# Optimization experiments

Measured on AMD Instinct MI355X. Metric: run time of the kernel, lower is better.

The kernel has to match this reference:

```python
import jax, jax.numpy as jnp
import numpy as np

T, B = 128, 512
OBS_DIM = 512
HIDDEN = 512
ACTION_DIM = 18
LN_EPS = 1e-6  # flax LayerNorm default


def _layer_norm(x, scale, bias):
    m = jnp.mean(x, axis=-1, keepdims=True)
    v = jnp.var(x, axis=-1, keepdims=True)
    return (x - m) * jax.lax.rsqrt(v + LN_EPS) * scale + bias


def setup_inputs() -> dict:
    key = jax.random.key(0)
    ks = jax.random.split(key, 16)
    sc = lambda k, sh: jax.random.normal(k, sh, jnp.float32) * (1.0 / np.sqrt(sh[0]))
    d = {}
    d['hidden'] = jax.random.normal(ks[0], (B, HIDDEN), jnp.float32)
    d['obs'] = jax.random.normal(ks[1], (T, B, OBS_DIM), jnp.float32)
    d['dones'] = jax.random.randint(ks[2], (T, B), 0, 2).astype(bool)
    d['last_acts'] = jax.random.randint(ks[3], (T, B), 0, ACTION_DIM, dtype=jnp.int32)
    in0 = OBS_DIM + ACTION_DIM
    d['w0'] = sc(ks[4], (in0, HIDDEN)); d['b0'] = jnp.zeros((HIDDEN,), jnp.float32)
    d['ln0_s'] = jnp.ones((HIDDEN,), jnp.float32); d['ln0_b'] = jnp.zeros((HIDDEN,), jnp.float32)
    d['w1'] = sc(ks[5], (HIDDEN, HIDDEN)); d['b1'] = jnp.zeros((HIDDEN,), jnp.float32)
    d['ln1_s'] = jnp.ones((HIDDEN,), jnp.float32); d['ln1_b'] = jnp.zeros((HIDDEN,), jnp.float32)
    d['w_ir'] = sc(ks[6], (HIDDEN, HIDDEN)); d['b_ir'] = jnp.zeros((HIDDEN,), jnp.float32)
    d['w_iz'] = sc(ks[7], (HIDDEN, HIDDEN)); d['b_iz'] = jnp.zeros((HIDDEN,), jnp.float32)
    d['w_in'] = sc(ks[8], (HIDDEN, HIDDEN)); d['b_in'] = jnp.zeros((HIDDEN,), jnp.float32)
    d['w_hr'] = sc(ks[9], (HIDDEN, HIDDEN))
    d['w_hz'] = sc(ks[10], (HIDDEN, HIDDEN))
    d['w_hn'] = sc(ks[11], (HIDDEN, HIDDEN)); d['b_hn'] = jnp.zeros((HIDDEN,), jnp.float32)
    d['w_out'] = sc(ks[12], (HIDDEN, ACTION_DIM)); d['b_out'] = jnp.zeros((ACTION_DIM,), jnp.float32)
    return d


def reference(hidden, obs, dones, last_acts,
              w0, b0, ln0_s, ln0_b, w1, b1, ln1_s, ln1_b,
              w_ir, b_ir, w_iz, b_iz, w_in, b_in,
              w_hr, w_hz, w_hn, b_hn, w_out, b_out):
    # embed last actions and concat with obs: [T, B, obs_dim + action_dim]
    one_hot = jax.nn.one_hot(last_acts, ACTION_DIM, dtype=obs.dtype)
    x = jnp.concatenate([obs, one_hot], axis=-1)
    # MLP encoder: Dense -> LayerNorm -> relu, applied over all (T, B) at once
    x = jax.nn.relu(_layer_norm(x @ w0 + b0, ln0_s, ln0_b))
    x = jax.nn.relu(_layer_norm(x @ w1 + b1, ln1_s, ln1_b))

    # ScannedRNN: GRUCell with reset-to-zero carry on done, scanned over time
    def step(h, xs):
        xt, dt = xs  # xt: [B, H], dt: [B] bool
        h = jnp.where(dt[:, None], jnp.zeros_like(h), h)
        r = jax.nn.sigmoid(xt @ w_ir + b_ir + h @ w_hr)
        z = jax.nn.sigmoid(xt @ w_iz + b_iz + h @ w_hz)
        n = jnp.tanh(xt @ w_in + b_in + r * (h @ w_hn + b_hn))
        h_new = (1.0 - z) * n + z * h
        return h_new, h_new

    new_hidden, y = jax.lax.scan(step, hidden, (x, dones))
    q_vals = y @ w_out + b_out  # [T, B, action_dim]
    return new_hidden, q_vals
```

## Files before the change

### kernel.cpp

```cpp
#include <hip/hip_runtime.h>
#include <cstdint>
#include <cstddef>


#define TT 128
#define BBATCH 512
#define HH 512
#define MM 65536
#define AD 18

typedef __attribute__((ext_vector_type(8))) short short8;
typedef __attribute__((ext_vector_type(4))) float float4v;
typedef __attribute__((ext_vector_type(4))) unsigned int uint4v;

__device__ __forceinline__ unsigned short f2bf(float f) {
  union { float f; unsigned int u; } v; v.f = f;
  unsigned int r = v.u + 0x7fffu + ((v.u >> 16) & 1u);
  return (unsigned short)(r >> 16);
}
__device__ __forceinline__ float bf2f(unsigned short h) {
  union { unsigned int u; float f; } v; v.u = ((unsigned int)h) << 16;
  return v.f;
}

__device__ __forceinline__ unsigned int load_u32_coh(const unsigned int* p) {
  unsigned int v;
  asm volatile("global_load_dword %0, %1, off sc0 sc1\n\ts_waitcnt vmcnt(0)"
               : "=v"(v) : "v"(p) : "memory");
  return v;
}
__device__ __forceinline__ void store_u32_coh(unsigned int* p, unsigned int v) {
  asm volatile("global_store_dword %0, %1, off sc0 sc1"
               :: "v"(p), "v"(v) : "memory");
}
__device__ __forceinline__ void store_u16_coh(unsigned short* p, unsigned int v) {
  asm volatile("global_store_short %0, %1, off sc0 sc1"
               :: "v"(p), "v"(v) : "memory");
}

typedef __attribute__((address_space(3))) unsigned int* lds_u32p;
typedef const __attribute__((address_space(1))) unsigned int* glb_u32p;
__device__ __forceinline__ void async16(void* lds, const void* g) {
  __builtin_amdgcn_global_load_lds(
      (glb_u32p)(unsigned long long)g,
      (lds_u32p)(unsigned int)(unsigned long long)lds, 16, 0, 0);
}


__global__ __launch_bounds__(256) void k_conv_obs(
    const float* __restrict__ src, unsigned short* __restrict__ dst,
    unsigned int* __restrict__ flag) {
  if (blockIdx.x == 0 && threadIdx.x == 0) *flag = 0u;
  int i = blockIdx.x * 256 + threadIdx.x;
  float4v v = ((const float4v*)src)[i];
  unsigned long long pk = (unsigned long long)f2bf(v[0])
      | ((unsigned long long)f2bf(v[1]) << 16)
      | ((unsigned long long)f2bf(v[2]) << 32)
      | ((unsigned long long)f2bf(v[3]) << 48);
  ((unsigned long long*)dst)[i] = pk;
}

__global__ __launch_bounds__(256) void k_prep_t(
    const float* __restrict__ w0, const float* __restrict__ w1,
    const float* __restrict__ wir, const float* __restrict__ wiz,
    const float* __restrict__ win,
    unsigned short* __restrict__ W0at, unsigned short* __restrict__ W1t,
    unsigned short* __restrict__ Wit) {
  int o = blockIdx.x * 256 + threadIdx.x;
  int n = o >> 9, k = o & 511;
  int z = blockIdx.y;
  const float* s = (z == 0) ? w0 : (z == 1) ? w1 : (z == 2) ? wir
                 : (z == 3) ? wiz : win;
  unsigned short b = f2bf(s[k * 512 + n]);
  if (z == 0) W0at[o] = b;
  else if (z == 1) W1t[o] = b;
  else Wit[(size_t)(z - 2) * 262144 + o] = b;
}

__global__ __launch_bounds__(256) void k_prep_whf(
    const float* __restrict__ whr, const float* __restrict__ whz,
    const float* __restrict__ whn, unsigned short* __restrict__ Whf) {
  int i = blockIdx.x * 256 + threadIdx.x;
  int k = i / 1536, n = i - k * 1536;
  const float* s = (n < 512) ? whr : (n < 1024) ? whz : whn;
  float v = s[k * 512 + (n & 511)];
  Whf[((size_t)(k >> 3) * 1536 + n) * 8 + (k & 7)] = f2bf(v);
}

__global__ __launch_bounds__(256) void k_prep_misc(
    const float* __restrict__ w0, const float* __restrict__ bir,
    const float* __restrict__ biz, const float* __restrict__ bin,
    const float* __restrict__ wout, const float* __restrict__ hidden,
    const int* __restrict__ dI,
    unsigned short* __restrict__ w0act, float* __restrict__ gib,
    unsigned short* __restrict__ WoutT, unsigned short* __restrict__ hbuf,
    unsigned int* __restrict__ ready, unsigned int* __restrict__ flag) {
  int i = blockIdx.x * 256 + threadIdx.x;
  if (i < 9216) {
    int a = i >> 9, n = i & 511;
    w0act[i] = f2bf(w0[(512 + a) * 512 + n]);
  }
  if (i < 1536)
    gib[i] = (i < 512) ? bir[i] : (i < 1024) ? biz[i - 512] : bin[i - 1024];
  if (i < 32768) {
    int n = i >> 9, k = i & 511;
    WoutT[i] = f2bf(n < AD ? wout[k * AD + n] : 0.f);
  }
  if (i < 262144) hbuf[i] = f2bf(hidden[i]);
  if (i < 33280) ready[i] = 0u;
  if (i < 16384) { if (dI[i] & 0xFFFFFFFE) atomicOr(flag, 1u); }
}


template <int MODE>
__global__ __launch_bounds__(256) void k_gemm_bt(
    const unsigned short* __restrict__ Ab,
    const unsigned short* __restrict__ Btb,
    unsigned short* __restrict__ Cb,
    int Ndim, const float* __restrict__ bias,
    const unsigned short* __restrict__ gW,
    const int* __restrict__ acts) {
  __shared__ unsigned short As[4096];
  __shared__ unsigned short Bs[4096];
  const int tid = threadIdx.x, wave = tid >> 6, lane = tid & 63;
  const int quad = lane >> 4, l15 = lane & 15;
  const int m0 = blockIdx.x * 128, n0 = blockIdx.y * 128;
  const int mblk = (wave & 1) * 64, nblk = (wave >> 1) * 64;

  float4v acc[4][4];
#pragma unroll
  for (int a = 0; a < 4; ++a)
#pragma unroll
    for (int b = 0; b < 4; ++b) acc[a][b] = (float4v){0.f, 0.f, 0.f, 0.f};

  for (int k0 = 0; k0 < 512; k0 += 32) {
#pragma unroll
    for (int r = 0; r < 2; ++r) {
      int u = r * 256 + wave * 64 + lane;
      int ch = u >> 7, mm = u & 127;
      async16(&As[(size_t)(r * 256 + wave * 64) * 8],
              Ab + (size_t)(m0 + mm) * 512 + k0 + ch * 8);
      async16(&Bs[(size_t)(r * 256 + wave * 64) * 8],
              Btb + (size_t)(n0 + mm) * 512 + k0 + ch * 8);
    }
    __syncthreads();
    short8 afr[4], bfr[4];
#pragma unroll
    for (int mi = 0; mi < 4; ++mi)
      afr[mi] = *(const short8*)&As[((quad << 7) + mblk + mi * 16 + l15) * 8];
#pragma unroll
    for (int ni = 0; ni < 4; ++ni)
      bfr[ni] = *(const short8*)&Bs[((quad << 7) + nblk + ni * 16 + l15) * 8];
#pragma unroll
    for (int mi = 0; mi < 4; ++mi)
#pragma unroll
      for (int ni = 0; ni < 4; ++ni)
        acc[mi][ni] = __builtin_amdgcn_mfma_f32_16x16x32_bf16(
            afr[mi], bfr[ni], acc[mi][ni], 0, 0, 0);
    __syncthreads();
  }

#pragma unroll
  for (int mi = 0; mi < 4; ++mi) {
#pragma unroll
    for (int i = 0; i < 4; ++i) {
      int row = m0 + mblk + mi * 16 + quad * 4 + i;
      int arow = (MODE == 1) ? acts[row] : 0;
#pragma unroll
      for (int ni = 0; ni < 4; ++ni) {
        int col = n0 + nblk + ni * 16 + l15;
        float v = acc[mi][ni][i] + bias[col];
        if (MODE == 1) v += bf2f(gW[arow * 512 + col]);
        Cb[(size_t)row * Ndim + col] = f2bf(v);
      }
    }
  }
}


__global__ __launch_bounds__(256) void k_ln_relu(
    const unsigned short* __restrict__ X, unsigned short* __restrict__ Y,
    const float* __restrict__ sc, const float* __restrict__ bi) {
  int row = blockIdx.x * 4 + (threadIdx.x >> 6);
  int lane = threadIdx.x & 63;
  uint4v u = *(const uint4v*)(X + (size_t)row * 512 + lane * 8);
  float v[8];
#pragma unroll
  for (int j = 0; j < 4; ++j) {
    v[2 * j] = bf2f((unsigned short)(u[j] & 0xffffu));
    v[2 * j + 1] = bf2f((unsigned short)(u[j] >> 16));
  }
  float s = 0.f, q = 0.f;
#pragma unroll
  for (int j = 0; j < 8; ++j) { s += v[j]; q += v[j] * v[j]; }
#pragma unroll
  for (int d = 1; d < 64; d <<= 1) {
    s += __shfl_xor(s, d, 64);
    q += __shfl_xor(q, d, 64);
  }
  float mean = s * (1.f / 512.f);
  float var = fmaxf(q * (1.f / 512.f) - mean * mean, 0.f);
  float rstd = rsqrtf(var + 1e-6f);
  float4v s0 = *(const float4v*)(sc + lane * 8);
  float4v s1 = *(const float4v*)(sc + lane * 8 + 4);
  float4v c0 = *(const float4v*)(bi + lane * 8);
  float4v c1 = *(const float4v*)(bi + lane * 8 + 4);
  uint4v w;
#pragma unroll
  for (int j = 0; j < 4; ++j) {
    float a0 = fmaxf((v[2 * j] - mean) * rstd * (j < 2 ? s0[2 * j] : s1[2 * j - 4])
                         + (j < 2 ? c0[2 * j] : c1[2 * j - 4]), 0.f);
    float a1 = fmaxf((v[2 * j + 1] - mean) * rstd
                         * (j < 2 ? s0[2 * j + 1] : s1[2 * j - 3])
                         + (j < 2 ? c0[2 * j + 1] : c1[2 * j - 3]), 0.f);
    w[j] = (unsigned int)f2bf(a0) | ((unsigned int)f2bf(a1) << 16);
  }
  *(uint4v*)(Y + (size_t)row * 512 + lane * 8) = w;
}


__global__ __launch_bounds__(256, 1) void k_gru(
    const unsigned short* __restrict__ Whf, const unsigned short* __restrict__ gin,
    const float* __restrict__ bhn, const int* __restrict__ dI,
    const unsigned char* __restrict__ dB, const unsigned int* __restrict__ flag,
    const unsigned short* __restrict__ hbuf, unsigned short* __restrict__ ybuf,
    float* __restrict__ outh, unsigned int* __restrict__ ready) {
  const int tid = threadIdx.x, wave = tid >> 6, lane = tid & 63;
  const int quad = lane >> 4, l15 = lane & 15;
  const int rt = blockIdx.x & 7;
  const int cc = blockIdx.x >> 3;
  const int r0 = rt * 64 + wave * 16;
  const int col = cc * 16 + l15;
  const int bytemode = (int)(*flag);
  const float bhn_c = bhn[col];

  short8 bw[3][16];
#pragma unroll
  for (int kc = 0; kc < 16; ++kc)
#pragma unroll
    for (int g = 0; g < 3; ++g) {
      size_t u = (size_t)(kc * 4 + quad) * 1536 + (g * 512 + col);
      bw[g][kc] = *(const short8*)(Whf + u * 8);
    }

  float hprev[4];
#pragma unroll
  for (int i = 0; i < 4; ++i) {
    int row = r0 + quad * 4 + i;
    hprev[i] = bf2f(hbuf[(size_t)row * 512 + col]);
  }

  const int myrowA = r0 + l15;

  float ginr[4], ginz[4], ginn[4];
  int dd[4], dA;
  {
    const unsigned short* gbase = gin;
#pragma unroll
    for (int i = 0; i < 4; ++i) {
      int row = r0 + quad * 4 + i;
      dd[i] = bytemode ? (int)dB[row] : dI[row];
      ginr[i] = bf2f(gbase[(size_t)row * 1536 + col]);
      ginz[i] = bf2f(gbase[(size_t)row * 1536 + 512 + col]);
      ginn[i] = bf2f(gbase[(size_t)row * 1536 + 1024 + col]);
    }
    dA = bytemode ? (int)dB[myrowA] : dI[myrowA];
  }

  for (int t = 0; t < TT; ++t) {
    if (t > 0) {
      if (wave == 0) {
        const unsigned int* fp =
            ready + ((size_t)rt * 130 + t) * 32 + (lane & 31);
        unsigned int v;
        int guard = 0;
        do {
          v = load_u32_coh(fp);
        } while (__ballot(v == 0u) != 0ull && ++guard < (1 << 22));
      }
      __syncthreads();
      asm volatile("" ::: "memory");
    }

    const unsigned short* hsrc =
        (t == 0) ? hbuf : ybuf + (size_t)(t - 1) * 262144;
    const unsigned short* ap = hsrc + (size_t)myrowA * 512 + quad * 8;
    short8 af[16];
#pragma unroll
    for (int kc = 0; kc < 16; ++kc) af[kc] = *(const short8*)(ap + kc * 32);
    if (dA) {
      const short8 z8 = {0, 0, 0, 0, 0, 0, 0, 0};
#pragma unroll
      for (int kc = 0; kc < 16; ++kc) af[kc] = z8;
    }

    float4v a0 = {0.f, 0.f, 0.f, 0.f}, a1 = a0, a2 = a0;
#pragma unroll
    for (int kc = 0; kc < 16; ++kc) {
      a0 = __builtin_amdgcn_mfma_f32_16x16x32_bf16(af[kc], bw[0][kc], a0, 0, 0, 0);
      a1 = __builtin_amdgcn_mfma_f32_16x16x32_bf16(af[kc], bw[1][kc], a1, 0, 0, 0);
      a2 = __builtin_amdgcn_mfma_f32_16x16x32_bf16(af[kc], bw[2][kc], a2, 0, 0, 0);
    }

    unsigned short* ydst = ybuf + (size_t)t * 262144;
#pragma unroll
    for (int i = 0; i < 4; ++i) {
      int row = r0 + quad * 4 + i;
      float hold = dd[i] ? 0.f : hprev[i];
      float r = 1.f / (1.f + __expf(-(a0[i] + ginr[i])));
      float z = 1.f / (1.f + __expf(-(a1[i] + ginz[i])));
      float npre = ginn[i] + r * (a2[i] + bhn_c);
      float n = 1.f - 2.f / (1.f + __expf(2.f * npre));
      float hnew = (1.f - z) * n + z * hold;
      hprev[i] = hnew;
      store_u16_coh(ydst + (size_t)row * 512 + col, (unsigned int)f2bf(hnew));
      if (t == TT - 1) outh[(size_t)row * 512 + col] = hnew;
    }

    __syncthreads();
    if (tid == 0)
      store_u32_coh(&ready[((size_t)rt * 130 + t + 1) * 32 + cc], 1u);

    if (t < TT - 1) {
      int tn = t + 1;
      const unsigned short* gbase = gin + (size_t)tn * 512 * 1536;
#pragma unroll
      for (int i = 0; i < 4; ++i) {
        int row = r0 + quad * 4 + i;
        dd[i] = bytemode ? (int)dB[tn * 512 + row] : dI[tn * 512 + row];
        ginr[i] = bf2f(gbase[(size_t)row * 1536 + col]);
        ginz[i] = bf2f(gbase[(size_t)row * 1536 + 512 + col]);
        ginn[i] = bf2f(gbase[(size_t)row * 1536 + 1024 + col]);
      }
      dA = bytemode ? (int)dB[tn * 512 + myrowA] : dI[tn * 512 + myrowA];
    }
  }
}


__global__ __launch_bounds__(256) void k_qout(
    const unsigned short* __restrict__ Yb, const unsigned short* __restrict__ Wt,
    const float* __restrict__ bout, float* __restrict__ Q) {
  __shared__ unsigned short As[4096];
  __shared__ unsigned short Bs[2048];
  const int tid = threadIdx.x, wave = tid >> 6, lane = tid & 63;
  const int quad = lane >> 4, l15 = lane & 15;
  const int m0 = blockIdx.x * 128;

  float4v acc[2][4];
#pragma unroll
  for (int a = 0; a < 2; ++a)
#pragma unroll
    for (int b = 0; b < 4; ++b) acc[a][b] = (float4v){0.f, 0.f, 0.f, 0.f};

  for (int k0 = 0; k0 < 512; k0 += 32) {
#pragma unroll
    for (int r = 0; r < 2; ++r) {
      int u = r * 256 + wave * 64 + lane;
      int ch = u >> 7, mm = u & 127;
      async16(&As[(size_t)(r * 256 + wave * 64) * 8],
              Yb + (size_t)(m0 + mm) * 512 + k0 + ch * 8);
    }
    {
      int u = wave * 64 + lane;
      int ch = u >> 6, nn = u & 63;
      async16(&Bs[(size_t)(wave * 64) * 8], Wt + (size_t)nn * 512 + k0 + ch * 8);
    }
    __syncthreads();
    short8 afr[2], bfr[4];
#pragma unroll
    for (int mi = 0; mi < 2; ++mi)
      afr[mi] = *(const short8*)&As[((quad << 7) + wave * 32 + mi * 16 + l15) * 8];
#pragma unroll
    for (int ni = 0; ni < 4; ++ni)
      bfr[ni] = *(const short8*)&Bs[((quad << 6) + ni * 16 + l15) * 8];
#pragma unroll
    for (int mi = 0; mi < 2; ++mi)
#pragma unroll
      for (int ni = 0; ni < 4; ++ni)
        acc[mi][ni] = __builtin_amdgcn_mfma_f32_16x16x32_bf16(
            afr[mi], bfr[ni], acc[mi][ni], 0, 0, 0);
    __syncthreads();
  }
#pragma unroll
  for (int mi = 0; mi < 2; ++mi)
#pragma unroll
    for (int ni = 0; ni < 4; ++ni)
#pragma unroll
      for (int i = 0; i < 4; ++i) {
        int row = m0 + wave * 32 + mi * 16 + quad * 4 + i;
        int colq = ni * 16 + l15;
        if (colq < AD) Q[(size_t)row * AD + colq] = acc[mi][ni][i] + bout[colq];
      }
}


extern "C" void kernel_launch(void* const* d_in, const int* in_sizes, int n_in,
                              void* d_out, int out_size, void* d_ws,
                              size_t ws_size, hipStream_t stream) {
  const float* hidden = (const float*)d_in[0];
  const float* obs = (const float*)d_in[1];
  const void* dones = d_in[2];
  const int* acts = (const int*)d_in[3];
  const float* w0 = (const float*)d_in[4];
  const float* b0 = (const float*)d_in[5];
  const float* ln0s = (const float*)d_in[6];
  const float* ln0b = (const float*)d_in[7];
  const float* w1 = (const float*)d_in[8];
  const float* b1 = (const float*)d_in[9];
  const float* ln1s = (const float*)d_in[10];
  const float* ln1b = (const float*)d_in[11];
  const float* wir = (const float*)d_in[12];
  const float* bir = (const float*)d_in[13];
  const float* wiz = (const float*)d_in[14];
  const float* biz = (const float*)d_in[15];
  const float* win = (const float*)d_in[16];
  const float* bin = (const float*)d_in[17];
  const float* whr = (const float*)d_in[18];
  const float* whz = (const float*)d_in[19];
  const float* whn = (const float*)d_in[20];
  const float* bhn = (const float*)d_in[21];
  const float* wout = (const float*)d_in[22];
  const float* bout = (const float*)d_in[23];

  char* ws = (char*)d_ws;
  unsigned short* bufA = (unsigned short*)(ws);
  unsigned short* bufB = (unsigned short*)(ws + 67108864ULL);
  unsigned short* gin = (unsigned short*)(ws + 134217728ULL);
  char* D = ws + 134217728ULL + 201326592ULL;
  unsigned short* W0at = (unsigned short*)(D);
  unsigned short* W1t = (unsigned short*)(D + 524288);
  unsigned short* Wit = (unsigned short*)(D + 1048576);
  unsigned short* Whf = (unsigned short*)(D + 2621440);
  unsigned short* WoutT = (unsigned short*)(D + 4194304);
  unsigned short* w0act = (unsigned short*)(D + 4259840);
  float* gib = (float*)(D + 4292608);
  unsigned short* hbuf = (unsigned short*)(D + 4300800);
  unsigned int* ready = (unsigned int*)(D + 5349376);
  unsigned int* flag = ready + 33280;

  (void)in_sizes; (void)n_in; (void)out_size; (void)ws_size;

  k_conv_obs<<<32768, 256, 0, stream>>>(obs, bufA, flag);
  k_prep_t<<<dim3(1024, 5), 256, 0, stream>>>(w0, w1, wir, wiz, win, W0at, W1t, Wit);
  k_prep_whf<<<3072, 256, 0, stream>>>(whr, whz, whn, Whf);
  k_prep_misc<<<1024, 256, 0, stream>>>(w0, bir, biz, bin, wout, hidden,
                                        (const int*)dones, w0act, gib, WoutT,
                                        hbuf, ready, flag);
  k_gemm_bt<1><<<dim3(512, 4), 256, 0, stream>>>(bufA, W0at, bufB, 512, b0, w0act, acts);
  k_ln_relu<<<16384, 256, 0, stream>>>(bufB, bufA, ln0s, ln0b);
  k_gemm_bt<0><<<dim3(512, 4), 256, 0, stream>>>(bufA, W1t, bufB, 512, b1, nullptr, nullptr);
  k_ln_relu<<<16384, 256, 0, stream>>>(bufB, bufA, ln1s, ln1b);
  k_gemm_bt<0><<<dim3(512, 12), 256, 0, stream>>>(bufA, Wit, gin, 1536, gib, nullptr, nullptr);
  k_gru<<<256, 256, 0, stream>>>(Whf, gin, bhn, (const int*)dones,
                                 (const unsigned char*)dones, flag, hbuf, bufB,
                                 (float*)d_out, ready);
  k_qout<<<512, 256, 0, stream>>>(bufB, WoutT, bout, (float*)d_out + 262144);
}
```

Measured before the change: 1.363 ms.

## Stage GRU input gates into LDS asynchronously and transpose MFMA for packed stores

```diff
diff --git a/kernel.cpp b/kernel.cpp
--- a/kernel.cpp
+++ b/kernel.cpp
@@ -8,6 +8,7 @@
 #define HH 512
 #define MM 65536
 #define AD 18
+#define GSTEPS 4
 
 typedef __attribute__((ext_vector_type(8))) short short8;
 typedef __attribute__((ext_vector_type(4))) float float4v;
@@ -33,8 +34,8 @@
   asm volatile("global_store_dword %0, %1, off sc0 sc1"
                :: "v"(p), "v"(v) : "memory");
 }
-__device__ __forceinline__ void store_u16_coh(unsigned short* p, unsigned int v) {
-  asm volatile("global_store_short %0, %1, off sc0 sc1"
+__device__ __forceinline__ void store_u64_coh(void* p, unsigned long long v) {
+  asm volatile("global_store_dwordx2 %0, %1, off sc0 sc1"
                :: "v"(p), "v"(v) : "memory");
 }
 
@@ -225,47 +226,64 @@
     const unsigned char* __restrict__ dB, const unsigned int* __restrict__ flag,
     const unsigned short* __restrict__ hbuf, unsigned short* __restrict__ ybuf,
     float* __restrict__ outh, unsigned int* __restrict__ ready) {
+  __shared__ __align__(16) unsigned short gin_lds[2][GSTEPS * 3 * 64 * 16];
+  __shared__ unsigned char d_lds[TT * 64];
+
   const int tid = threadIdx.x, wave = tid >> 6, lane = tid & 63;
   const int quad = lane >> 4, l15 = lane & 15;
   const int rt = blockIdx.x & 7;
   const int cc = blockIdx.x >> 3;
-  const int r0 = rt * 64 + wave * 16;
-  const int col = cc * 16 + l15;
+  const int r0b = rt * 64;
+  const int rowb = wave * 16 + l15;
+  const int row = r0b + rowb;
+  const int c0 = cc * 16 + quad * 4;
   const int bytemode = (int)(*flag);
-  const float bhn_c = bhn[col];
+  const float4v bhn4 = *(const float4v*)(bhn + c0);
+
+  auto stage_gin = [&](int buf, int t0) {
+#pragma unroll
+    for (int r = 0; r < 6; ++r) {
+      int u = r * 256 + tid;
+      int half = u & 1;
+      int v = u >> 1;
+      int rr = v & 63;
+      int v2 = v >> 6;
+      int g = v2 % 3, s = v2 / 3;
+      const unsigned short* src = gin
+          + ((size_t)(t0 + s) * 512 + r0b + rr) * 1536 + g * 512 + cc * 16
+          + half * 8;
+      async16(&gin_lds[buf][(size_t)(r * 256 + wave * 64) * 8], src);
+    }
+  };
+
+  stage_gin(0, 0);
+#pragma unroll
+  for (int r = 0; r < 32; ++r) {
+    int idx = r * 256 + tid;
+    int t = idx >> 6, rr = idx & 63;
+    int gidx = t * 512 + r0b + rr;
+    d_lds[idx] = bytemode ? dB[gidx] : (unsigned char)(dI[gidx] != 0);
+  }
 
   short8 bw[3][16];
 #pragma unroll
   for (int kc = 0; kc < 16; ++kc)
 #pragma unroll
     for (int g = 0; g < 3; ++g) {
-      size_t u = (size_t)(kc * 4 + quad) * 1536 + (g * 512 + col);
+      size_t u = (size_t)(kc * 4 + quad) * 1536 + (g * 512 + cc * 16 + l15);
       bw[g][kc] = *(const short8*)(Whf + u * 8);
     }
 
   float hprev[4];
-#pragma unroll
-  for (int i = 0; i < 4; ++i) {
-    int row = r0 + quad * 4 + i;
-    hprev[i] = bf2f(hbuf[(size_t)row * 512 + col]);
-  }
-
-  const int myrowA = r0 + l15;
-
-  float ginr[4], ginz[4], ginn[4];
-  int dd[4], dA;
   {
-    const unsigned short* gbase = gin;
-#pragma unroll
-    for (int i = 0; i < 4; ++i) {
-      int row = r0 + quad * 4 + i;
-      dd[i] = bytemode ? (int)dB[row] : dI[row];
-      ginr[i] = bf2f(gbase[(size_t)row * 1536 + col]);
-      ginz[i] = bf2f(gbase[(size_t)row * 1536 + 512 + col]);
-      ginn[i] = bf2f(gbase[(size_t)row * 1536 + 1024 + col]);
-    }
-    dA = bytemode ? (int)dB[myrowA] : dI[myrowA];
-  }
+    unsigned long long w = *(const unsigned long long*)(hbuf + (size_t)row * 512 + c0);
+#pragma unroll
+    for (int i = 0; i < 4; ++i) hprev[i] = bf2f((unsigned short)(w >> (16 * i)));
+  }
+
+  __syncthreads();
+
+  const unsigned short* apOffBase = nullptr;  (void)apOffBase;
 
   for (int t = 0; t < TT; ++t) {
     if (t > 0) {
@@ -284,56 +302,72 @@
 
     const unsigned short* hsrc =
         (t == 0) ? hbuf : ybuf + (size_t)(t - 1) * 262144;
-    const unsigned short* ap = hsrc + (size_t)myrowA * 512 + quad * 8;
+    const unsigned short* ap = hsrc + (size_t)row * 512 + quad * 8;
     short8 af[16];
 #pragma unroll
     for (int kc = 0; kc < 16; ++kc) af[kc] = *(const short8*)(ap + kc * 32);
-    if (dA) {
+
+    const int dd = (int)d_lds[(t << 6) + rowb];
+    if (dd) {
       const short8 z8 = {0, 0, 0, 0, 0, 0, 0, 0};
 #pragma unroll
       for (int kc = 0; kc < 16; ++kc) af[kc] = z8;
     }
 
+    if ((t & (GSTEPS - 1)) == 0 && t + GSTEPS < TT)
+      stage_gin(((t >> 2) + 1) & 1, t + GSTEPS);
+
+    const int sl = t & (GSTEPS - 1), bufc = (t >> 2) & 1;
+    float gr[4], gz[4], gn[4];
+    {
+      const unsigned short* gl =
+          &gin_lds[bufc][((size_t)(sl * 3) * 64 + rowb) * 16 + quad * 4];
+      unsigned long long w0 = *(const unsigned long long*)(gl);
+      unsigned long long w1 = *(const unsigned long long*)(gl + 1024);
+      unsigned long long w2 = *(const unsigned long long*)(gl + 2048);
+#pragma unroll
+      for (int i = 0; i < 4; ++i) {
+        gr[i] = bf2f((unsigned short)(w0 >> (16 * i)));
+        gz[i] = bf2f((unsigned short)(w1 >> (16 * i)));
+        gn[i] = bf2f((unsigned short)(w2 >> (16 * i)));
+      }
+    }
+
     float4v a0 = {0.f, 0.f, 0.f, 0.f}, a1 = a0, a2 = a0;
 #pragma unroll
     for (int kc = 0; kc < 16; ++kc) {
-      a0 = __builtin_amdgcn_mfma_f32_16x16x32_bf16(af[kc], bw[0][kc], a0, 0, 0, 0);
-      a1 = __builtin_amdgcn_mfma_f32_16x16x32_bf16(af[kc], bw[1][kc], a1, 0, 0, 0);
-      a2 = __builtin_amdgcn_mfma_f32_16x16x32_bf16(af[kc], bw[2][kc], a2, 0, 0, 0);
+      a0 = __builtin_amdgcn_mfma_f32_16x16x32_bf16(bw[0][kc], af[kc], a0, 0, 0, 0);
+      a1 = __builtin_amdgcn_mfma_f32_16x16x32_bf16(bw[1][kc], af[kc], a1, 0, 0, 0);
+      a2 = __builtin_amdgcn_mfma_f32_16x16x32_bf16(bw[2][kc], af[kc], a2, 0, 0, 0);
     }
 
     unsigned short* ydst = ybuf + (size_t)t * 262144;
+    float hv[4];
 #pragma unroll
     for (int i = 0; i < 4; ++i) {
-      int row = r0 + quad * 4 + i;
-      float hold = dd[i] ? 0.f : hprev[i];
-      float r = 1.f / (1.f + __expf(-(a0[i] + ginr[i])));
-      float z = 1.f / (1.f + __expf(-(a1[i] + ginz[i])));
-      float npre = ginn[i] + r * (a2[i] + bhn_c);
+      float hold = dd ? 0.f : hprev[i];
+      float r = 1.f / (1.f + __expf(-(a0[i] + gr[i])));
+      float z = 1.f / (1.f + __expf(-(a1[i] + gz[i])));
+      float npre = gn[i] + r * (a2[i] + bhn4[i]);
       float n = 1.f - 2.f / (1.f + __expf(2.f * npre));
-      float hnew = (1.f - z) * n + z * hold;
-      hprev[i] = hnew;
-      store_u16_coh(ydst + (size_t)row * 512 + col, (unsigned int)f2bf(hnew));
-      if (t == TT - 1) outh[(size_t)row * 512 + col] = hnew;
+      hv[i] = (1.f - z) * n + z * hold;
+      hprev[i] = hv[i];
+    }
+    {
+      unsigned long long pk = (unsigned long long)f2bf(hv[0])
+          | ((unsigned long long)f2bf(hv[1]) << 16)
+          | ((unsigned long long)f2bf(hv[2]) << 32)
+          | ((unsigned long long)f2bf(hv[3]) << 48);
+      store_u64_coh(ydst + (size_t)row * 512 + c0, pk);
+    }
+    if (t == TT - 1) {
+      float4v o = {hv[0], hv[1], hv[2], hv[3]};
+      *(float4v*)(outh + (size_t)row * 512 + c0) = o;
     }
 
     __syncthreads();
     if (tid == 0)
       store_u32_coh(&ready[((size_t)rt * 130 + t + 1) * 32 + cc], 1u);
-
-    if (t < TT - 1) {
-      int tn = t + 1;
-      const unsigned short* gbase = gin + (size_t)tn * 512 * 1536;
-#pragma unroll
-      for (int i = 0; i < 4; ++i) {
-        int row = r0 + quad * 4 + i;
-        dd[i] = bytemode ? (int)dB[tn * 512 + row] : dI[tn * 512 + row];
-        ginr[i] = bf2f(gbase[(size_t)row * 1536 + col]);
-        ginz[i] = bf2f(gbase[(size_t)row * 1536 + 512 + col]);
-        ginn[i] = bf2f(gbase[(size_t)row * 1536 + 1024 + col]);
-      }
-      dA = bytemode ? (int)dB[tn * 512 + myrowA] : dI[tn * 512 + myrowA];
-    }
   }
 }
 
```

Result: faster. 1.312 ms (-3.8%).
